# Kernel optimization log

Measured on AMD Instinct MI355X. Metric: run time of the kernel, lower is better.

## Reference

```python
import jax, jax.numpy as jnp
import numpy as np

KERNEL_LEN = 128
INPUT_LEN = 1_000_000
MAX_PATH = 30          # hardcoded self.max_path in the module
PATH_NUM = 10          # self.path_num / out_len
L = INPUT_LEN + KERNEL_LEN  # max possible DTW path length


def setup_inputs() -> dict:
    key = jax.random.key(0)
    k1, k2, k3, k4, k5 = jax.random.split(key, 5)
    kernel = jax.random.normal(k1, (KERNEL_LEN,), dtype=jnp.float32)
    x = jax.random.normal(k2, (INPUT_LEN,), dtype=jnp.float32)
    # path indices produced by the external DP library (opaque int outputs)
    path_k = jax.random.randint(k3, (MAX_PATH, L), 0, KERNEL_LEN, dtype=jnp.int32)
    path_i = jax.random.randint(k4, (MAX_PATH, L), 0, INPUT_LEN, dtype=jnp.int32)
    path_length = jax.random.randint(k5, (MAX_PATH,), 0, L, dtype=jnp.int32)
    return {"kernel": kernel, "x": x, "path_k": path_k, "path_i": path_i,
            "path_length": path_length, "path_num": 12}


def reference(kernel, x, path_k, path_i, path_length, path_num):
    # out[k] = sum_{i < path_length[k]} (kernel[path_k[k,i]] - x[path_i[k,i]])**2
    # for k < min(path_num, PATH_NUM); remaining entries stay zero.
    n = min(int(path_num), PATH_NUM)
    pk = path_k[:PATH_NUM]                      # [PATH_NUM, L]
    pi = path_i[:PATH_NUM]
    step_mask = jnp.arange(L)[None, :] < path_length[:PATH_NUM, None]  # ragged lengths
    diff = kernel[pk] - x[pi]                   # gather + elementwise, [PATH_NUM, L]
    sq = jnp.where(step_mask, diff * diff, jnp.float32(0))
    out = sq.sum(axis=1)                        # [PATH_NUM]
    k_mask = jnp.arange(PATH_NUM) < n
    return jnp.where(k_mask, out, jnp.float32(0))
```

## Files before the change

kernel.cpp:

```cpp
#include <hip/hip_runtime.h>

#define KERNEL_LEN 128
#define INPUT_LEN 1000000
#define PATH_NUM 10
#define L_TOTAL (INPUT_LEN + KERNEL_LEN)
#define NBLOCKS 2048
#define BLOCK_SIZE 256
#define CHUNK 4

typedef int v4i __attribute__((ext_vector_type(4)));

__global__ __launch_bounds__(BLOCK_SIZE) void dtw_spring_npath_kernel(
    const float* __restrict__ kern,
    const float* __restrict__ x,
    const int*   __restrict__ path_k,
    const int*   __restrict__ path_i,
    const int*   __restrict__ path_length,
    const int*   __restrict__ path_num,
    float*       __restrict__ out)
{
    __shared__ float k_lds[KERNEL_LEN];
    const int tid = threadIdx.x;
    if (tid < KERNEL_LEN) k_lds[tid] = kern[tid];
    __syncthreads();

    const int n = min(path_num[0], PATH_NUM);

    float acc[PATH_NUM];
    #pragma unroll
    for (int p = 0; p < PATH_NUM; ++p) acc[p] = 0.0f;

    const int start  = (blockIdx.x * BLOCK_SIZE + tid) * CHUNK;
    const int stride = NBLOCKS * BLOCK_SIZE * CHUNK;

    #pragma unroll
    for (int p = 0; p < PATH_NUM; ++p) {
        if (p < n) {
            const int len  = path_length[p];
            const int len4 = len & ~(CHUNK - 1);
            const int* __restrict__ pk = path_k + (size_t)p * L_TOTAL;
            const int* __restrict__ pi = path_i + (size_t)p * L_TOTAL;

            float a = 0.0f;
            for (int t = start; t < len4; t += stride) {
                const v4i ik = *reinterpret_cast<const v4i*>(pk + t);
                const v4i ii = *reinterpret_cast<const v4i*>(pi + t);
                const float x0 = x[(unsigned)ii[0]];
                const float x1 = x[(unsigned)ii[1]];
                const float x2 = x[(unsigned)ii[2]];
                const float x3 = x[(unsigned)ii[3]];
                const float d0 = k_lds[(unsigned)ik[0]] - x0;
                const float d1 = k_lds[(unsigned)ik[1]] - x1;
                const float d2 = k_lds[(unsigned)ik[2]] - x2;
                const float d3 = k_lds[(unsigned)ik[3]] - x3;
                a = fmaf(d0, d0, a);
                a = fmaf(d1, d1, a);
                a = fmaf(d2, d2, a);
                a = fmaf(d3, d3, a);
            }
            if (blockIdx.x == 0) {
                const int t = len4 + tid;
                if (t < len) {
                    const float d = k_lds[pk[t]] - x[pi[t]];
                    a = fmaf(d, d, a);
                }
            }
            acc[p] = a;
        }
    }

    __shared__ float wsum[PATH_NUM][BLOCK_SIZE / 64];
    const int wave = tid >> 6;
    const int lane = tid & 63;
    #pragma unroll
    for (int p = 0; p < PATH_NUM; ++p) {
        float a = acc[p];
        #pragma unroll
        for (int off = 32; off > 0; off >>= 1)
            a += __shfl_down(a, off, 64);
        if (lane == 0) wsum[p][wave] = a;
    }
    __syncthreads();
    if (tid < PATH_NUM && tid < n) {
        const float s = wsum[tid][0] + wsum[tid][1] + wsum[tid][2] + wsum[tid][3];
        if (s != 0.0f) atomicAdd(&out[tid], s);
    }
}

extern "C" void kernel_launch(void* const* d_in, const int* in_sizes, int n_in,
                              void* d_out, int out_size, void* d_ws, size_t ws_size,
                              hipStream_t stream) {
    const float* kern        = (const float*)d_in[0];
    const float* x           = (const float*)d_in[1];
    const int*   path_k      = (const int*)d_in[2];
    const int*   path_i      = (const int*)d_in[3];
    const int*   path_length = (const int*)d_in[4];
    const int*   path_num    = (const int*)d_in[5];
    float*       out         = (float*)d_out;

    hipMemsetAsync(out, 0, (size_t)out_size * sizeof(float), stream);

    dtw_spring_npath_kernel<<<dim3(NBLOCKS), dim3(BLOCK_SIZE), 0, stream>>>(
        kern, x, path_k, path_i, path_length, path_num, out);
}
```

Before: 53.83 us.

## Split x gathers into two index-range passes and replace atomics with two-stage reduction

Measured after the change: 64.98 us. 20.7% more time.

```diff
diff --git a/kernel.cpp b/kernel.cpp
--- a/kernel.cpp
+++ b/kernel.cpp
@@ -7,17 +7,19 @@
 #define NBLOCKS 2048
 #define BLOCK_SIZE 256
 #define CHUNK 4
+#define NPASS 2
+#define SLICE (INPUT_LEN / NPASS)
 
 typedef int v4i __attribute__((ext_vector_type(4)));
 
-__global__ __launch_bounds__(BLOCK_SIZE) void dtw_spring_npath_kernel(
+__global__ __launch_bounds__(BLOCK_SIZE) void dtw_partials(
     const float* __restrict__ kern,
     const float* __restrict__ x,
     const int*   __restrict__ path_k,
     const int*   __restrict__ path_i,
     const int*   __restrict__ path_length,
     const int*   __restrict__ path_num,
-    float*       __restrict__ out)
+    float*       __restrict__ ws)
 {
     __shared__ float k_lds[KERNEL_LEN];
     const int tid = threadIdx.x;
@@ -33,39 +35,41 @@
     const int start  = (blockIdx.x * BLOCK_SIZE + tid) * CHUNK;
     const int stride = NBLOCKS * BLOCK_SIZE * CHUNK;
 
-    #pragma unroll
-    for (int p = 0; p < PATH_NUM; ++p) {
-        if (p < n) {
-            const int len  = path_length[p];
-            const int len4 = len & ~(CHUNK - 1);
-            const int* __restrict__ pk = path_k + (size_t)p * L_TOTAL;
-            const int* __restrict__ pi = path_i + (size_t)p * L_TOTAL;
+    for (int pass = 0; pass < NPASS; ++pass) {
+        const unsigned base = pass * SLICE;
+        #pragma unroll
+        for (int p = 0; p < PATH_NUM; ++p) {
+            if (p < n) {
+                const int len  = path_length[p];
+                const int len4 = len & ~(CHUNK - 1);
+                const int* __restrict__ pk = path_k + (size_t)p * L_TOTAL;
+                const int* __restrict__ pi = path_i + (size_t)p * L_TOTAL;
 
-            float a = 0.0f;
-            for (int t = start; t < len4; t += stride) {
-                const v4i ik = *reinterpret_cast<const v4i*>(pk + t);
-                const v4i ii = *reinterpret_cast<const v4i*>(pi + t);
-                const float x0 = x[(unsigned)ii[0]];
-                const float x1 = x[(unsigned)ii[1]];
-                const float x2 = x[(unsigned)ii[2]];
-                const float x3 = x[(unsigned)ii[3]];
-                const float d0 = k_lds[(unsigned)ik[0]] - x0;
-                const float d1 = k_lds[(unsigned)ik[1]] - x1;
-                const float d2 = k_lds[(unsigned)ik[2]] - x2;
-                const float d3 = k_lds[(unsigned)ik[3]] - x3;
-                a = fmaf(d0, d0, a);
-                a = fmaf(d1, d1, a);
-                a = fmaf(d2, d2, a);
-                a = fmaf(d3, d3, a);
+                float a = 0.0f;
+                for (int t = start; t < len4; t += stride) {
+                    const v4i ik = *reinterpret_cast<const v4i*>(pk + t);
+                    const v4i ii = *reinterpret_cast<const v4i*>(pi + t);
+                    #pragma unroll
+                    for (int j = 0; j < 4; ++j) {
+                        const unsigned r = (unsigned)ii[j] - base;
+                        if (r < SLICE) {
+                            const float d = k_lds[(unsigned)ik[j]] - x[base + r];
+                            a = fmaf(d, d, a);
+                        }
+                    }
+                }
+                if (blockIdx.x == 0) {
+                    const int t = len4 + tid;
+                    if (t < len) {
+                        const unsigned r = (unsigned)pi[t] - base;
+                        if (r < SLICE) {
+                            const float d = k_lds[pk[t]] - x[base + r];
+                            a = fmaf(d, d, a);
+                        }
+                    }
+                }
+                acc[p] += a;
             }
-            if (blockIdx.x == 0) {
-                const int t = len4 + tid;
-                if (t < len) {
-                    const float d = k_lds[pk[t]] - x[pi[t]];
-                    a = fmaf(d, d, a);
-                }
-            }
-            acc[p] = a;
         }
     }
 
@@ -81,9 +85,45 @@
         if (lane == 0) wsum[p][wave] = a;
     }
     __syncthreads();
-    if (tid < PATH_NUM && tid < n) {
+    if (tid < PATH_NUM) {
         const float s = wsum[tid][0] + wsum[tid][1] + wsum[tid][2] + wsum[tid][3];
-        if (s != 0.0f) atomicAdd(&out[tid], s);
+        ws[(size_t)tid * NBLOCKS + blockIdx.x] = (tid < n) ? s : 0.0f;
+    }
+}
+
+__global__ __launch_bounds__(BLOCK_SIZE) void dtw_reduce(
+    const float* __restrict__ ws,
+    const int*   __restrict__ path_num,
+    float*       __restrict__ out)
+{
+    const int tid = threadIdx.x;
+    const int n = min(path_num[0], PATH_NUM);
+
+    float acc[PATH_NUM];
+    #pragma unroll
+    for (int p = 0; p < PATH_NUM; ++p) acc[p] = 0.0f;
+
+    for (int t = tid; t < NBLOCKS; t += BLOCK_SIZE) {
+        #pragma unroll
+        for (int p = 0; p < PATH_NUM; ++p)
+            acc[p] += ws[(size_t)p * NBLOCKS + t];
+    }
+
+    __shared__ float wsum[PATH_NUM][BLOCK_SIZE / 64];
+    const int wave = tid >> 6;
+    const int lane = tid & 63;
+    #pragma unroll
+    for (int p = 0; p < PATH_NUM; ++p) {
+        float a = acc[p];
+        #pragma unroll
+        for (int off = 32; off > 0; off >>= 1)
+            a += __shfl_down(a, off, 64);
+        if (lane == 0) wsum[p][wave] = a;
+    }
+    __syncthreads();
+    if (tid < PATH_NUM) {
+        const float s = wsum[tid][0] + wsum[tid][1] + wsum[tid][2] + wsum[tid][3];
+        out[tid] = (tid < n) ? s : 0.0f;
     }
 }
 
@@ -97,9 +137,10 @@
     const int*   path_length = (const int*)d_in[4];
     const int*   path_num    = (const int*)d_in[5];
     float*       out         = (float*)d_out;
+    float*       partials    = (float*)d_ws;
 
-    hipMemsetAsync(out, 0, (size_t)out_size * sizeof(float), stream);
-
-    dtw_spring_npath_kernel<<<dim3(NBLOCKS), dim3(BLOCK_SIZE), 0, stream>>>(
-        kern, x, path_k, path_i, path_length, path_num, out);
+    dtw_partials<<<dim3(NBLOCKS), dim3(BLOCK_SIZE), 0, stream>>>(
+        kern, x, path_k, path_i, path_length, path_num, partials);
+    dtw_reduce<<<dim3(1), dim3(BLOCK_SIZE), 0, stream>>>(
+        partials, path_num, out);
 }
```

## Map each block to one fixed window per path with rotated window assignment

Applied to the files above, without the earlier changes.

New measurement: 52.45 us. 2.6% less time.

```diff
diff --git a/kernel.cpp b/kernel.cpp
--- a/kernel.cpp
+++ b/kernel.cpp
@@ -4,9 +4,11 @@
 #define INPUT_LEN 1000000
 #define PATH_NUM 10
 #define L_TOTAL (INPUT_LEN + KERNEL_LEN)
-#define NBLOCKS 2048
 #define BLOCK_SIZE 256
 #define CHUNK 4
+#define CHUNK_ELEMS (BLOCK_SIZE * CHUNK)
+#define NWIN 977
+#define WIN_ROT 98
 
 typedef int v4i __attribute__((ext_vector_type(4)));
 
@@ -24,27 +26,26 @@
     if (tid < KERNEL_LEN) k_lds[tid] = kern[tid];
     __syncthreads();
 
-    const int n = min(path_num[0], PATH_NUM);
+    const int n   = min(path_num[0], PATH_NUM);
+    const int bid = blockIdx.x;
 
     float acc[PATH_NUM];
     #pragma unroll
     for (int p = 0; p < PATH_NUM; ++p) acc[p] = 0.0f;
 
-    const int start  = (blockIdx.x * BLOCK_SIZE + tid) * CHUNK;
-    const int stride = NBLOCKS * BLOCK_SIZE * CHUNK;
-
     #pragma unroll
     for (int p = 0; p < PATH_NUM; ++p) {
         if (p < n) {
-            const int len  = path_length[p];
-            const int len4 = len & ~(CHUNK - 1);
-            const int* __restrict__ pk = path_k + (size_t)p * L_TOTAL;
-            const int* __restrict__ pi = path_i + (size_t)p * L_TOTAL;
-
-            float a = 0.0f;
-            for (int t = start; t < len4; t += stride) {
-                const v4i ik = *reinterpret_cast<const v4i*>(pk + t);
-                const v4i ii = *reinterpret_cast<const v4i*>(pi + t);
+            const int len = path_length[p];
+            int w = bid + p * WIN_ROT;
+            if (w >= NWIN) w -= NWIN;
+            if (w * CHUNK_ELEMS < len) {
+                const int t0 = w * CHUNK_ELEMS + tid * CHUNK;
+                const int tl = min(t0, L_TOTAL - CHUNK);
+                const int* __restrict__ pk = path_k + (size_t)p * L_TOTAL;
+                const int* __restrict__ pi = path_i + (size_t)p * L_TOTAL;
+                const v4i ik = *reinterpret_cast<const v4i*>(pk + tl);
+                const v4i ii = *reinterpret_cast<const v4i*>(pi + tl);
                 const float x0 = x[(unsigned)ii[0]];
                 const float x1 = x[(unsigned)ii[1]];
                 const float x2 = x[(unsigned)ii[2]];
@@ -53,19 +54,13 @@
                 const float d1 = k_lds[(unsigned)ik[1]] - x1;
                 const float d2 = k_lds[(unsigned)ik[2]] - x2;
                 const float d3 = k_lds[(unsigned)ik[3]] - x3;
-                a = fmaf(d0, d0, a);
-                a = fmaf(d1, d1, a);
-                a = fmaf(d2, d2, a);
-                a = fmaf(d3, d3, a);
+                float a = 0.0f;
+                a = fmaf(d0, d0, a); a = (t0 + 0 < len) ? a : 0.0f;
+                float b1 = fmaf(d1, d1, 0.0f); a += (t0 + 1 < len) ? b1 : 0.0f;
+                float b2 = fmaf(d2, d2, 0.0f); a += (t0 + 2 < len) ? b2 : 0.0f;
+                float b3 = fmaf(d3, d3, 0.0f); a += (t0 + 3 < len) ? b3 : 0.0f;
+                acc[p] += a;
             }
-            if (blockIdx.x == 0) {
-                const int t = len4 + tid;
-                if (t < len) {
-                    const float d = k_lds[pk[t]] - x[pi[t]];
-                    a = fmaf(d, d, a);
-                }
-            }
-            acc[p] = a;
         }
     }
 
@@ -100,6 +95,6 @@
 
     hipMemsetAsync(out, 0, (size_t)out_size * sizeof(float), stream);
 
-    dtw_spring_npath_kernel<<<dim3(NBLOCKS), dim3(BLOCK_SIZE), 0, stream>>>(
+    dtw_spring_npath_kernel<<<dim3(NWIN), dim3(BLOCK_SIZE), 0, stream>>>(
         kern, x, path_k, path_i, path_length, path_num, out);
 }
```
